# Performance work log

Measured on AMD Instinct MI355X. Metric: run time of the kernel, lower is better.

Reference implementation:

```python
import jax, jax.numpy as jnp
import numpy as np

TAGSET = 256
NUM_TAGS = TAGSET + 2
START, END = TAGSET, TAGSET + 1
PAD = -1
B, S = 128, 1024


def setup_inputs() -> dict:
    key = jax.random.key(0)
    k1, k2, k3 = jax.random.split(key, 3)
    logits = jax.random.normal(k1, (B, S, TAGSET), dtype=jnp.float32)
    y = jax.random.randint(k2, (B, S), 0, TAGSET)
    # variable sequence lengths; tail padded with tag_pad_id = -1
    lengths = jax.random.randint(k3, (B,), S // 2, S + 1)
    y = jnp.where(jnp.arange(S)[None, :] < lengths[:, None], y, PAD).astype(jnp.int64)
    # transitions parameter, initialized as in CRF_Loss.__init__
    transitions = jnp.full((NUM_TAGS, NUM_TAGS), -np.log(NUM_TAGS), dtype=jnp.float32)
    transitions = transitions.at[END, :].set(-10000.0)
    transitions = transitions.at[:, START].set(-10000.0)
    return {"logits": logits, "transitions": transitions, "y": y}


def _crf_loss(logits, transitions, y):
    mask = (y != PAD).astype(logits.dtype)  # [B,S]
    s_lens = mask.sum(1)

    # ---- log Z: forward (alpha) recurrence over time via lax.scan ----
    trans_tt = transitions[:START, :START]  # [T,T]
    log_alpha = logits[:, 0] + transitions[START, :START][None, :]  # [B,T]

    def step(la, inp):
        em, m = inp  # em: [B,T], m: [B]
        # score[b,j] = logsumexp_i( la[b,i] + trans[i,j] + em[b,j] )
        score = jax.nn.logsumexp(la[:, :, None] + trans_tt[None] + em[:, None, :], axis=1)
        la = jnp.where(m[:, None] > 0, score, la)
        return la, None

    ems = jnp.swapaxes(logits[:, 1:], 0, 1)  # [S-1,B,T]
    ms = jnp.swapaxes(mask[:, 1:], 0, 1)     # [S-1,B]
    log_alpha, _ = jax.lax.scan(step, log_alpha, (ems, ms))
    log_z = jax.nn.logsumexp(log_alpha + transitions[:START, END][None, :], axis=1)  # [B]

    # ---- gold-path score log p(Y|X) numerator (vectorized over time) ----
    tags = jnp.where(y < 0, 0, y)  # clamp pads to a valid index
    llh = transitions[START, tags[:, 0]]
    llh = llh + jnp.take_along_axis(logits[:, 0], tags[:, 0:1], axis=1)[:, 0] * mask[:, 0]
    em_sc = jnp.take_along_axis(logits[:, 1:], tags[:, 1:, None], axis=2)[..., 0]  # [B,S-1]
    tr_sc = transitions[tags[:, :-1], tags[:, 1:]]                                  # [B,S-1]
    llh = llh + jnp.sum((em_sc + tr_sc) * mask[:, 1:], axis=1)
    last_idx = s_lens.astype(jnp.int32) - 1
    last_tags = jnp.take_along_axis(tags, last_idx[:, None], axis=1)[:, 0]
    llh = llh + transitions[last_tags, END]

    loss = -(llh - log_z) / s_lens
    return loss.mean()


def reference(logits, transitions, y):
    return _crf_loss(logits, transitions, y)
```

## Files before the change

### kernel.cpp

```cpp
#include <hip/hip_runtime.h>

#define B_   128
#define S_   1024
#define NT_  258
#define TG_  256
#define LN2f 0.69314718056f
#define RSTR 264
#define BUF  (16*RSTR)

typedef __attribute__((ext_vector_type(8))) short bf8_t;
typedef __attribute__((ext_vector_type(4))) float f4_t;

__device__ __forceinline__ unsigned short f2bf(float f) {
  unsigned u = __float_as_uint(f);
  u += 0x7fffu + ((u >> 16) & 1u);
  return (unsigned short)(u >> 16);
}
__device__ __forceinline__ float bf2f(unsigned short s) {
  return __uint_as_float(((unsigned)s) << 16);
}
__device__ __forceinline__ unsigned pk_bf16(float lo, float hi) {
  unsigned d;
  asm("v_cvt_pk_bf16_f32 %0, %1, %2" : "=v"(d) : "v"(lo), "v"(hi));
  return d;
}

__global__ __launch_bounds__(512, 2) void crf_scan(
    const float* __restrict__ logits, const float* __restrict__ trans,
    const int* __restrict__ y, float* __restrict__ ws)
{
  __shared__ __align__(16) unsigned short aL[2*BUF];
  __shared__ __align__(16) int   earr[16];
  __shared__ float esumL[16];
  __shared__ float refL[16];

  const int tid = threadIdx.x;
  const int w  = tid >> 6;
  const int l  = tid & 63;
  const int bq = blockIdx.x * 16;
  const int lg = l >> 4;
  const int lc = l & 15;

  bf8_t Bf0[8], Bf1[8];
#pragma unroll
  for (int kk = 0; kk < 8; ++kk) {
    bf8_t b0, b1;
    const int n = 32*w + 2*lc;
#pragma unroll
    for (int e = 0; e < 8; ++e) {
      const int k = kk*32 + lg*8 + e;
      b0[e] = (short)f2bf(__expf(trans[k*NT_ + n]));
      b1[e] = (short)f2bf(__expf(trans[k*NT_ + n + 1]));
    }
    Bf0[kk] = b0; Bf1[kk] = b1;
  }

  const int idxA0 = lc*RSTR + lg*8;
  int idxW_r[4], embase_r[4], ybase[4];
#pragma unroll
  for (int r = 0; r < 4; ++r) {
    const int b = 4*lg + r;
    idxW_r[r]   = b*RSTR + 32*w + 2*lc;
    embase_r[r] = (bq + b)*(S_*256) + 32*w + 2*lc;
    ybase[r]    = (bq + b)*S_;
  }

  {
    if (tid < 16) {
      refL[tid]  = logits[(size_t)(bq + tid)*(S_*256)] + trans[TG_*NT_];
      esumL[tid] = 0.f;
    }
    __syncthreads();
    const int bi = tid >> 5;
    const int cb = (tid & 31) * 8;
    const float ref = refL[bi];
    uint2 dd;
    {
      const float4 em = *(const float4*)&logits[(size_t)(bq + bi)*(S_*256) + cb];
      const float4 ts = *(const float4*)&trans[TG_*NT_ + cb];
      dd.x = pk_bf16(__expf(em.x + ts.x - ref), __expf(em.y + ts.y - ref));
      dd.y = pk_bf16(__expf(em.z + ts.z - ref), __expf(em.w + ts.w - ref));
    }
    *(uint2*)&aL[bi*RSTR + cb] = dd;
    {
      const float4 em = *(const float4*)&logits[(size_t)(bq + bi)*(S_*256) + cb + 4];
      const float4 ts = *(const float4*)&trans[TG_*NT_ + cb + 4];
      dd.x = pk_bf16(__expf(em.x + ts.x - ref), __expf(em.y + ts.y - ref));
      dd.y = pk_bf16(__expf(em.z + ts.z - ref), __expf(em.w + ts.w - ref));
    }
    *(uint2*)&aL[bi*RSTR + cb + 4] = dd;
  }

  float2 emA[4], emB[4];
  int yA[4], yB[4];
#pragma unroll
  for (int r = 0; r < 4; ++r) {
    yA[r] = y[ybase[r] + 1];
    yB[r] = y[ybase[r] + 2];
    emA[r] = *(const float2*)&logits[embase_r[r] + 1*256];
    emB[r] = *(const float2*)&logits[embase_r[r] + 2*256];
  }
  float esv[4] = {0.f, 0.f, 0.f, 0.f};

  __syncthreads();

#define SCAN_STEP(T_, CURE_, NXTE_, EMV_, YV_) do {                           \
  bf8_t Af_[8];                                                               \
  _Pragma("unroll") for (int kk = 0; kk < 8; ++kk)                            \
    Af_[kk] = *(const bf8_t*)&aL[(CURE_) + idxA0 + 32*kk];                    \
  float F0_[4], F1_[4]; int m_[4];                                            \
  _Pragma("unroll") for (int r = 0; r < 4; ++r) {                             \
    m_[r] = YV_[r];                                                           \
    F0_[r] = __expf(EMV_[r].x); F1_[r] = __expf(EMV_[r].y); }                 \
  const int tp_ = ((T_)+2 < S_) ? ((T_)+2) : (S_-1);                          \
  _Pragma("unroll") for (int r = 0; r < 4; ++r) {                             \
    YV_[r] = y[ybase[r] + tp_];                                               \
    EMV_[r] = *(const float2*)&logits[embase_r[r] + tp_*256]; }               \
  f4_t c0_ = {0.f,0.f,0.f,0.f}, c1_ = {0.f,0.f,0.f,0.f};                      \
  _Pragma("unroll") for (int kk = 0; kk < 8; ++kk) {                          \
    c0_ = __builtin_amdgcn_mfma_f32_16x16x32_bf16(Af_[kk], Bf0[kk], c0_, 0, 0, 0); \
    c1_ = __builtin_amdgcn_mfma_f32_16x16x32_bf16(Af_[kk], Bf1[kk], c1_, 0, 0, 0); } \
  float v0_[4], v1_[4];                                                       \
  _Pragma("unroll") for (int r = 0; r < 4; ++r) {                             \
    v0_[r] = F0_[r]*c0_[r]; v1_[r] = F1_[r]*c1_[r]; }                         \
  if (((T_) & 7) == 0) {                    \
    const int4 er_ = *(const int4*)&earr[lg*4];                               \
    v0_[0] = ldexpf(v0_[0], -er_.x); v1_[0] = ldexpf(v1_[0], -er_.x);         \
    v0_[1] = ldexpf(v0_[1], -er_.y); v1_[1] = ldexpf(v1_[1], -er_.y);         \
    v0_[2] = ldexpf(v0_[2], -er_.z); v1_[2] = ldexpf(v1_[2], -er_.z);         \
    v0_[3] = ldexpf(v0_[3], -er_.w); v1_[3] = ldexpf(v1_[3], -er_.w);         \
    if (w == 0 && lc == 0) {                                                  \
      if (m_[0] >= 0) esv[0] += (float)er_.x;                                 \
      if (m_[1] >= 0) esv[1] += (float)er_.y;                                 \
      if (m_[2] >= 0) esv[2] += (float)er_.z;                                 \
      if (m_[3] >= 0) esv[3] += (float)er_.w; } }                             \
  _Pragma("unroll") for (int r = 0; r < 4; ++r) {                             \
    unsigned d_ = pk_bf16(v0_[r], v1_[r]);                                    \
    const unsigned old_ = *(const unsigned*)&aL[(CURE_) + idxW_r[r]];         \
    if (m_[r] < 0) d_ = old_;               \
    *(unsigned*)&aL[(NXTE_) + idxW_r[r]] = d_; }                              \
  if (((T_) & 7) == 7 && w == 0 && lc == 0) {   \
    _Pragma("unroll") for (int r = 0; r < 4; ++r)                             \
      earr[4*lg + r] = (int)((__float_as_uint(v0_[r]) >> 23) & 255) - 127; }  \
  asm volatile("s_waitcnt lgkmcnt(0)" ::: "memory");   \
  __builtin_amdgcn_s_barrier();                        \
  asm volatile("" ::: "memory");                       \
} while (0)

  SCAN_STEP(1, 0, BUF, emA, yA);
#pragma unroll 1
  for (int tt = 2; tt < S_; tt += 2) {
    SCAN_STEP(tt,   BUF, 0, emB, yB);
    SCAN_STEP(tt+1, 0, BUF, emA, yA);
  }
#undef SCAN_STEP

  if (w == 0 && lc == 0) {
#pragma unroll
    for (int r = 0; r < 4; ++r) esumL[4*lg + r] = esv[r];
  }
  __syncthreads();
  {
    const int bi = tid >> 5, j0 = (tid & 31) * 8;
    float p = 0.f;
#pragma unroll
    for (int e = 0; e < 8; ++e) {
      const int k = j0 + e;
      p += bf2f(aL[BUF + bi*RSTR + k]) * __expf(trans[k*NT_ + 257]);
    }
#pragma unroll
    for (int o = 16; o; o >>= 1) p += __shfl_xor(p, o, 32);
    if ((tid & 31) == 0)
      ws[128 + bq + bi] = __logf(p) + esumL[bi]*LN2f + refL[bi];
  }
}

__global__ void crf_llh(const float* __restrict__ logits, const float* __restrict__ trans,
                        const int* __restrict__ y, float* __restrict__ ws)
{
  const int b = blockIdx.x, tid = threadIdx.x;
  const int yb = b * S_;
  float part = 0.f; int cnt = 0;
  for (int t = tid; t < S_; t += 256) {
    const int yt = y[yb + t];
    const bool m = (yt >= 0);
    if (m) ++cnt;
    if (t == 0) {
      const int tag0 = m ? yt : 0;
      part += trans[TG_*NT_ + tag0];
      if (m) part += logits[(size_t)yb * 256 + tag0];
    } else if (m) {
      const int yp = y[yb + t - 1];
      part += logits[((size_t)(yb + t)) * 256 + yt] + trans[yp*NT_ + yt];
    }
    if (m && (t + 1 == S_ || y[yb + t + 1] < 0))
      part += trans[yt*NT_ + 257];
  }
#pragma unroll
  for (int o = 32; o; o >>= 1) { part += __shfl_xor(part, o); cnt += __shfl_xor(cnt, o); }
  __shared__ float sp[4]; __shared__ int sc[4];
  if ((tid & 63) == 0) { sp[tid >> 6] = part; sc[tid >> 6] = cnt; }
  __syncthreads();
  if (tid == 0) {
    ws[b]       = sp[0] + sp[1] + sp[2] + sp[3];
    ws[256 + b] = (float)(sc[0] + sc[1] + sc[2] + sc[3]);
  }
}

__global__ void crf_fin(const float* __restrict__ ws, float* __restrict__ out)
{
  const int i = threadIdx.x;
  float v = -(ws[i] - ws[128 + i]) / ws[256 + i];
#pragma unroll
  for (int o = 32; o; o >>= 1) v += __shfl_xor(v, o);
  __shared__ float s2[2];
  if ((i & 63) == 0) s2[i >> 6] = v;
  __syncthreads();
  if (i == 0) out[0] = (s2[0] + s2[1]) * (1.0f / 128.0f);
}

extern "C" void kernel_launch(void* const* d_in, const int* in_sizes, int n_in,
                              void* d_out, int out_size, void* d_ws, size_t ws_size,
                              hipStream_t stream)
{
  const float* logits = (const float*)d_in[0];
  const float* trans  = (const float*)d_in[1];
  const int*   y      = (const int*)d_in[2];
  float* ws  = (float*)d_ws;
  float* out = (float*)d_out;

  hipLaunchKernelGGL(crf_llh,  dim3(128), dim3(256), 0, stream, logits, trans, y, ws);
  hipLaunchKernelGGL(crf_scan, dim3(8),   dim3(512), 0, stream, logits, trans, y, ws);
  hipLaunchKernelGGL(crf_fin,  dim3(1),   dim3(128), 0, stream, ws, out);
}
```

Baseline: 683.9 us.

## Split CRF forward scan across 32 blocks of 4 sequences each

The forward-recurrence kernel now handles 4 batch rows per block instead of 16, launching 32 blocks instead of 8 so more compute units run the latency-bound sequential scan. The MFMA A-operand rows are replicated by mapping the 16 MFMA rows onto 4 real sequences, so only lane group 0 writes back results. This spreads the per-step wave work and LDS traffic across more CUs, at the cost of wasting three quarters of each MFMA and reloading the transition matrix into registers in four times as many blocks.

```diff
diff --git a/kernel.cpp b/kernel.cpp
--- a/kernel.cpp
+++ b/kernel.cpp
@@ -1,12 +1,11 @@
 #include <hip/hip_runtime.h>
 
-#define B_   128
-#define S_   1024
-#define NT_  258
-#define TG_  256
-#define LN2f 0.69314718056f
-#define RSTR 264
-#define BUF  (16*RSTR)
+#define S_    1024
+#define NT_   258
+#define TG_   256
+#define LN2f  0.69314718056f
+#define RSTR4 272
+#define BUF4  (4*RSTR4)
 
 typedef __attribute__((ext_vector_type(8))) short bf8_t;
 typedef __attribute__((ext_vector_type(4))) float f4_t;
@@ -16,8 +15,8 @@
   u += 0x7fffu + ((u >> 16) & 1u);
   return (unsigned short)(u >> 16);
 }
-__device__ __forceinline__ float bf2f(unsigned short s) {
-  return __uint_as_float(((unsigned)s) << 16);
+__device__ __forceinline__ float bf2f(unsigned s) {
+  return __uint_as_float(s << 16);
 }
 __device__ __forceinline__ unsigned pk_bf16(float lo, float hi) {
   unsigned d;
@@ -25,19 +24,19 @@
   return d;
 }
 
-__global__ __launch_bounds__(512, 2) void crf_scan(
+__global__ __launch_bounds__(512, 2) void crf_scan4(
     const float* __restrict__ logits, const float* __restrict__ trans,
     const int* __restrict__ y, float* __restrict__ ws)
 {
-  __shared__ __align__(16) unsigned short aL[2*BUF];
-  __shared__ __align__(16) int   earr[16];
-  __shared__ float esumL[16];
-  __shared__ float refL[16];
+  __shared__ __align__(16) unsigned short aL[2*BUF4];
+  __shared__ __align__(16) int   earr[4];
+  __shared__ float esumL[4];
+  __shared__ float refL[4];
 
   const int tid = threadIdx.x;
   const int w  = tid >> 6;
   const int l  = tid & 63;
-  const int bq = blockIdx.x * 16;
+  const int bq = blockIdx.x * 4;
   const int lg = l >> 4;
   const int lc = l & 15;
 
@@ -55,40 +54,41 @@
     Bf0[kk] = b0; Bf1[kk] = b1;
   }
 
-  const int idxA0 = lc*RSTR + lg*8;
+  const int idxA0 = (lc & 3)*RSTR4 + lg*8;
   int idxW_r[4], embase_r[4], ybase[4];
 #pragma unroll
   for (int r = 0; r < 4; ++r) {
-    const int b = 4*lg + r;
-    idxW_r[r]   = b*RSTR + 32*w + 2*lc;
-    embase_r[r] = (bq + b)*(S_*256) + 32*w + 2*lc;
-    ybase[r]    = (bq + b)*S_;
+    idxW_r[r]   = r*RSTR4 + 32*w + 2*lc;
+    embase_r[r] = (bq + r)*(S_*256) + 32*w + 2*lc;
+    ybase[r]    = (bq + r)*S_;
   }
 
   {
-    if (tid < 16) {
+    if (tid < 4) {
       refL[tid]  = logits[(size_t)(bq + tid)*(S_*256)] + trans[TG_*NT_];
       esumL[tid] = 0.f;
     }
     __syncthreads();
-    const int bi = tid >> 5;
-    const int cb = (tid & 31) * 8;
-    const float ref = refL[bi];
-    uint2 dd;
-    {
-      const float4 em = *(const float4*)&logits[(size_t)(bq + bi)*(S_*256) + cb];
-      const float4 ts = *(const float4*)&trans[TG_*NT_ + cb];
-      dd.x = pk_bf16(__expf(em.x + ts.x - ref), __expf(em.y + ts.y - ref));
-      dd.y = pk_bf16(__expf(em.z + ts.z - ref), __expf(em.w + ts.w - ref));
-    }
-    *(uint2*)&aL[bi*RSTR + cb] = dd;
-    {
-      const float4 em = *(const float4*)&logits[(size_t)(bq + bi)*(S_*256) + cb + 4];
-      const float4 ts = *(const float4*)&trans[TG_*NT_ + cb + 4];
-      dd.x = pk_bf16(__expf(em.x + ts.x - ref), __expf(em.y + ts.y - ref));
-      dd.y = pk_bf16(__expf(em.z + ts.z - ref), __expf(em.w + ts.w - ref));
-    }
-    *(uint2*)&aL[bi*RSTR + cb + 4] = dd;
+    if (tid < 128) {
+      const int bi = tid >> 5;
+      const int cb = (tid & 31) * 8;
+      const float ref = refL[bi];
+      uint2 dd;
+      {
+        const float4 em = *(const float4*)&logits[(size_t)(bq + bi)*(S_*256) + cb];
+        const float4 ts = *(const float4*)&trans[TG_*NT_ + cb];
+        dd.x = pk_bf16(__expf(em.x + ts.x - ref), __expf(em.y + ts.y - ref));
+        dd.y = pk_bf16(__expf(em.z + ts.z - ref), __expf(em.w + ts.w - ref));
+      }
+      *(uint2*)&aL[bi*RSTR4 + cb] = dd;
+      {
+        const float4 em = *(const float4*)&logits[(size_t)(bq + bi)*(S_*256) + cb + 4];
+        const float4 ts = *(const float4*)&trans[TG_*NT_ + cb + 4];
+        dd.x = pk_bf16(__expf(em.x + ts.x - ref), __expf(em.y + ts.y - ref));
+        dd.y = pk_bf16(__expf(em.z + ts.z - ref), __expf(em.w + ts.w - ref));
+      }
+      *(uint2*)&aL[bi*RSTR4 + cb + 4] = dd;
+    }
   }
 
   float2 emA[4], emB[4];
@@ -123,50 +123,50 @@
   float v0_[4], v1_[4];                                                       \
   _Pragma("unroll") for (int r = 0; r < 4; ++r) {                             \
     v0_[r] = F0_[r]*c0_[r]; v1_[r] = F1_[r]*c1_[r]; }                         \
-  if (((T_) & 7) == 0) {                    \
-    const int4 er_ = *(const int4*)&earr[lg*4];                               \
+  if (((T_) & 7) == 0) {                     \
+    const int4 er_ = *(const int4*)&earr[0];                                  \
     v0_[0] = ldexpf(v0_[0], -er_.x); v1_[0] = ldexpf(v1_[0], -er_.x);         \
     v0_[1] = ldexpf(v0_[1], -er_.y); v1_[1] = ldexpf(v1_[1], -er_.y);         \
     v0_[2] = ldexpf(v0_[2], -er_.z); v1_[2] = ldexpf(v1_[2], -er_.z);         \
     v0_[3] = ldexpf(v0_[3], -er_.w); v1_[3] = ldexpf(v1_[3], -er_.w);         \
-    if (w == 0 && lc == 0) {                                                  \
+    if (w == 0 && l == 0) {                                                   \
       if (m_[0] >= 0) esv[0] += (float)er_.x;                                 \
       if (m_[1] >= 0) esv[1] += (float)er_.y;                                 \
       if (m_[2] >= 0) esv[2] += (float)er_.z;                                 \
       if (m_[3] >= 0) esv[3] += (float)er_.w; } }                             \
-  _Pragma("unroll") for (int r = 0; r < 4; ++r) {                             \
-    unsigned d_ = pk_bf16(v0_[r], v1_[r]);                                    \
-    const unsigned old_ = *(const unsigned*)&aL[(CURE_) + idxW_r[r]];         \
-    if (m_[r] < 0) d_ = old_;               \
-    *(unsigned*)&aL[(NXTE_) + idxW_r[r]] = d_; }                              \
-  if (((T_) & 7) == 7 && w == 0 && lc == 0) {   \
+  if (lg == 0) {                                   \
+    _Pragma("unroll") for (int r = 0; r < 4; ++r) {                           \
+      unsigned d_ = pk_bf16(v0_[r], v1_[r]);                                  \
+      const unsigned old_ = *(const unsigned*)&aL[(CURE_) + idxW_r[r]];       \
+      if (m_[r] < 0) d_ = old_;                  \
+      *(unsigned*)&aL[(NXTE_) + idxW_r[r]] = d_; } }                          \
+  if (((T_) & 7) == 7 && w == 0 && l == 0) {    \
     _Pragma("unroll") for (int r = 0; r < 4; ++r)                             \
-      earr[4*lg + r] = (int)((__float_as_uint(v0_[r]) >> 23) & 255) - 127; }  \
-  asm volatile("s_waitcnt lgkmcnt(0)" ::: "memory");   \
-  __builtin_amdgcn_s_barrier();                        \
-  asm volatile("" ::: "memory");                       \
+      earr[r] = (int)((__float_as_uint(v0_[r]) >> 23) & 255) - 127; }         \
+  asm volatile("s_waitcnt lgkmcnt(0)\n\ts_barrier" ::: "memory");             \
+  __builtin_amdgcn_sched_barrier(0);                                          \
 } while (0)
 
-  SCAN_STEP(1, 0, BUF, emA, yA);
+  SCAN_STEP(1, 0, BUF4, emA, yA);
 #pragma unroll 1
   for (int tt = 2; tt < S_; tt += 2) {
-    SCAN_STEP(tt,   BUF, 0, emB, yB);
-    SCAN_STEP(tt+1, 0, BUF, emA, yA);
+    SCAN_STEP(tt,   BUF4, 0, emB, yB);
+    SCAN_STEP(tt+1, 0, BUF4, emA, yA);
   }
 #undef SCAN_STEP
 
-  if (w == 0 && lc == 0) {
-#pragma unroll
-    for (int r = 0; r < 4; ++r) esumL[4*lg + r] = esv[r];
-  }
-  __syncthreads();
-  {
+  if (w == 0 && l == 0) {
+#pragma unroll
+    for (int r = 0; r < 4; ++r) esumL[r] = esv[r];
+  }
+  __syncthreads();
+  if (tid < 128) {
     const int bi = tid >> 5, j0 = (tid & 31) * 8;
     float p = 0.f;
 #pragma unroll
     for (int e = 0; e < 8; ++e) {
       const int k = j0 + e;
-      p += bf2f(aL[BUF + bi*RSTR + k]) * __expf(trans[k*NT_ + 257]);
+      p += bf2f(aL[BUF4 + bi*RSTR4 + k]) * __expf(trans[k*NT_ + 257]);
     }
 #pragma unroll
     for (int o = 16; o; o >>= 1) p += __shfl_xor(p, o, 32);
@@ -229,7 +229,7 @@
   float* ws  = (float*)d_ws;
   float* out = (float*)d_out;
 
-  hipLaunchKernelGGL(crf_llh,  dim3(128), dim3(256), 0, stream, logits, trans, y, ws);
-  hipLaunchKernelGGL(crf_scan, dim3(8),   dim3(512), 0, stream, logits, trans, y, ws);
-  hipLaunchKernelGGL(crf_fin,  dim3(1),   dim3(128), 0, stream, ws, out);
-}
+  hipLaunchKernelGGL(crf_llh,   dim3(128), dim3(256), 0, stream, logits, trans, y, ws);
+  hipLaunchKernelGGL(crf_scan4, dim3(32),  dim3(512), 0, stream, logits, trans, y, ws);
+  hipLaunchKernelGGL(crf_fin,   dim3(1),   dim3(128), 0, stream, ws, out);
+}
```

New measurement: 642.3 us. 6.1% less time.
